# Performance work log

Measured on AMD Instinct MI355X. Metric: run time of the kernel, lower is better.

The kernel has to match this reference:

```python
import jax, jax.numpy as jnp
import numpy as np

N, K, D = 50000, 32, 128


def setup_inputs() -> dict:
    key = jax.random.key(0)
    k1, k2, k3, k4 = jax.random.split(key, 4)
    v_fea = jax.random.normal(k1, (N, D), dtype=jnp.float32)
    t_emb = jax.random.normal(k2, (N, D), dtype=jnp.float32)
    ef = jax.random.randint(k3, (N, K), 0, N, dtype=jnp.int64)
    # nn.Linear(2D, 2D, bias=False) weight, scaled like torch default init
    W = jax.random.normal(k4, (2 * D, 2 * D), dtype=jnp.float32) * (1.0 / np.sqrt(2 * D))
    return {"v_fea": v_fea, "t_emb": t_emb, "ef": ef, "W": W}


def reference(v_fea, t_emb, ef, W):
    # v: gathered neighbor features [N, K, D]
    v = v_fea[ef]
    # q: [N, 2D]; torch Linear applies x @ W.T
    q = jnp.concatenate([v_fea, t_emb], axis=-1)
    wq = q @ W.T                                   # [N, 2D]
    # k: [N, K, 2D]
    k = jnp.concatenate([v, t_emb[ef]], axis=-1)
    # per-edge score: bmm(k, wq[..., None]) -> [N, K]
    r = jnp.einsum("nkd,nd->nk", k, wq)
    r = jax.nn.softmax(r, axis=1)                  # softmax over neighbors
    # weighted sum over neighbors -> [N, D]
    ef_fea = jnp.einsum("nk,nkd->nd", r, v)
    return ef_fea
```

## Files before the change

### kernel.cpp

```cpp
#include <hip/hip_runtime.h>
#include <hip/hip_bf16.h>

#define D     128
#define TWO_D 256
#define KNB   32

typedef __attribute__((ext_vector_type(8))) short    s8;
typedef __attribute__((ext_vector_type(8))) _Float16 h8;
typedef __attribute__((ext_vector_type(2))) _Float16 h2v;
typedef __attribute__((ext_vector_type(4))) float    f4;

__device__ inline unsigned short f2h(float f) {
    return __builtin_bit_cast(unsigned short, (_Float16)f);
}
__device__ inline float h2f(unsigned short u) {
    return (float)__builtin_bit_cast(_Float16, u);
}

union v16u { s8 s; h2v h[4]; };

__device__ inline float dot8(s8 x, s8 w, float acc) {
#if __has_builtin(__builtin_amdgcn_fdot2)
    v16u ux, uw; ux.s = x; uw.s = w;
#pragma unroll
    for (int j = 0; j < 4; ++j)
        acc = __builtin_amdgcn_fdot2(ux.h[j], uw.h[j], acc, false);
#else
#pragma unroll
    for (int j = 0; j < 8; ++j)
        acc = fmaf(h2f((unsigned short)x[j]), h2f((unsigned short)w[j]), acc);
#endif
    return acc;
}

__global__ __launch_bounds__(256) void cast_kernel(
    const float* __restrict__ a, const float* __restrict__ b,
    unsigned short* __restrict__ ph, int total)
{
    int i = blockIdx.x * 256 + threadIdx.x;
    if (i >= total) return;
    int n = i >> 4, j = i & 15;
    const float4* pv = (const float4*)(a + (size_t)n * D + j * 8);
    const float4* pt = (const float4*)(b + (size_t)n * D + j * 8);
    float4 v0 = pv[0], v1 = pv[1];
    float4 t0 = pt[0], t1 = pt[1];
    s8 qv, qt;
    qv[0]=(short)f2h(v0.x); qv[1]=(short)f2h(v0.y); qv[2]=(short)f2h(v0.z); qv[3]=(short)f2h(v0.w);
    qv[4]=(short)f2h(v1.x); qv[5]=(short)f2h(v1.y); qv[6]=(short)f2h(v1.z); qv[7]=(short)f2h(v1.w);
    qt[0]=(short)f2h(t0.x); qt[1]=(short)f2h(t0.y); qt[2]=(short)f2h(t0.z); qt[3]=(short)f2h(t0.w);
    qt[4]=(short)f2h(t1.x); qt[5]=(short)f2h(t1.y); qt[6]=(short)f2h(t1.z); qt[7]=(short)f2h(t1.w);
    *(s8*)(ph + (size_t)n * TWO_D + j * 8)     = qv;
    *(s8*)(ph + (size_t)n * TWO_D + D + j * 8) = qt;
}

#define BM 128
#define BN 128
#define BK 32
#define LDT 56

__global__ __launch_bounds__(256) void gemm_wq_mfma(
    const unsigned short* __restrict__ ph,
    const float* __restrict__ W, unsigned short* __restrict__ wq_h, int M)
{
    __shared__ unsigned short As[BM][LDT];
    __shared__ unsigned short Bs[BN][LDT];

    const int tid  = threadIdx.x;
    const int w    = tid >> 6;
    const int lane = tid & 63;
    const int quad = lane >> 4;
    const int l16  = lane & 15;
    const int row0 = blockIdx.x * BM;
    const int i0   = blockIdx.y * BN;

    f4 acc[2][8] = {};

    const int srow = tid >> 1;
    const int seg  = tid & 1;
    int ga = row0 + srow; if (ga >= M) ga = M - 1;

    for (int kt = 0; kt < TWO_D; kt += BK) {
        const unsigned short* pa = ph + (size_t)ga * TWO_D + kt + seg * 16;
        s8 a0 = *(const s8*)(pa);
        s8 a1 = *(const s8*)(pa + 8);
        const float* pb = W + (size_t)(i0 + srow) * TWO_D + kt + seg * 16;
        float4 b0 = *(const float4*)(pb);
        float4 b1 = *(const float4*)(pb + 4);
        float4 b2 = *(const float4*)(pb + 8);
        float4 b3 = *(const float4*)(pb + 12);

        __syncthreads();
        *(s8*)&As[srow][seg * 16]     = a0;
        *(s8*)&As[srow][seg * 16 + 8] = a1;
        {
            s8 q0, q1;
            q0[0]=(short)f2h(b0.x); q0[1]=(short)f2h(b0.y); q0[2]=(short)f2h(b0.z); q0[3]=(short)f2h(b0.w);
            q0[4]=(short)f2h(b1.x); q0[5]=(short)f2h(b1.y); q0[6]=(short)f2h(b1.z); q0[7]=(short)f2h(b1.w);
            q1[0]=(short)f2h(b2.x); q1[1]=(short)f2h(b2.y); q1[2]=(short)f2h(b2.z); q1[3]=(short)f2h(b2.w);
            q1[4]=(short)f2h(b3.x); q1[5]=(short)f2h(b3.y); q1[6]=(short)f2h(b3.z); q1[7]=(short)f2h(b3.w);
            *(s8*)&Bs[srow][seg * 16]     = q0;
            *(s8*)&Bs[srow][seg * 16 + 8] = q1;
        }
        __syncthreads();

        s8 af0 = *(const s8*)&As[w * 32 + l16][quad * 8];
        s8 af1 = *(const s8*)&As[w * 32 + 16 + l16][quad * 8];
#pragma unroll
        for (int nt = 0; nt < 8; ++nt) {
            s8 bf = *(const s8*)&Bs[nt * 16 + l16][quad * 8];
            acc[0][nt] = __builtin_amdgcn_mfma_f32_16x16x32_f16(
                __builtin_bit_cast(h8, af0), __builtin_bit_cast(h8, bf), acc[0][nt], 0, 0, 0);
            acc[1][nt] = __builtin_amdgcn_mfma_f32_16x16x32_f16(
                __builtin_bit_cast(h8, af1), __builtin_bit_cast(h8, bf), acc[1][nt], 0, 0, 0);
        }
    }

#pragma unroll
    for (int mt = 0; mt < 2; ++mt) {
#pragma unroll
        for (int nt = 0; nt < 8; ++nt) {
#pragma unroll
            for (int r = 0; r < 4; ++r) {
                int grow = row0 + w * 32 + mt * 16 + quad * 4 + r;
                if (grow < M)
                    wq_h[(size_t)grow * TWO_D + i0 + nt * 16 + l16] = f2h(acc[mt][nt][r]);
            }
        }
    }
}

__global__ __attribute__((amdgpu_waves_per_eu(4, 4))) __launch_bounds__(256)
void attn_kernel(
    const unsigned short* __restrict__ ph, const int* __restrict__ ef,
    const unsigned short* __restrict__ wq_h, float* __restrict__ outp, int M)
{
    const int lane = threadIdx.x & 63;
    const int w    = threadIdx.x >> 6;
    const int n    = blockIdx.x * 4 + w;
    if (n >= M) return;

    const int g = lane >> 4;
    const int j = lane & 15;

    const unsigned short* wp = wq_h + (size_t)n * TWO_D + j * 16;
    s8 wqa = *(const s8*)(wp);
    s8 wqb = *(const s8*)(wp + 8);

    int eidx = 0;
    if (lane < KNB) eidx = ef[n * KNB + lane];

    s8 xa[8], xb[8];
#pragma unroll
    for (int p = 0; p < 8; ++p) {
        int e = __shfl(eidx, 4 * p + g, 64);
        const unsigned short* rp = ph + (size_t)e * TWO_D + j * 16;
        xa[p] = *(const s8*)(rp);
        xb[p] = *(const s8*)(rp + 8);
    }
    __builtin_amdgcn_sched_barrier(0);

    float s[8];
#pragma unroll
    for (int p = 0; p < 8; ++p) {
        float t = dot8(xa[p], wqa, 0.f);
        s[p] = dot8(xb[p], wqb, t);
    }

#pragma unroll
    for (int p = 0; p < 8; ++p) {
#pragma unroll
        for (int off = 8; off; off >>= 1) s[p] += __shfl_xor(s[p], off, 64);
    }
    float m = -1e30f;
#pragma unroll
    for (int p = 0; p < 8; ++p) {
        float sb = __shfl_xor(s[p], 16, 64);
        float m2 = fmaxf(s[p], sb);
        float m3 = __shfl_xor(m2, 32, 64);
        m = fmaxf(m, fmaxf(m2, m3));
    }
    float e[8];
    float psum = 0.f;
#pragma unroll
    for (int p = 0; p < 8; ++p) {
        e[p] = __expf(s[p] - m);
        psum += e[p];
    }
    psum += __shfl_xor(psum, 16, 64);
    psum += __shfl_xor(psum, 32, 64);

    float o[16] = {};
#pragma unroll
    for (int p = 0; p < 8; ++p) {
        v16u ua, ub; ua.s = xa[p]; ub.s = xb[p];
#pragma unroll
        for (int t = 0; t < 4; ++t) {
            o[2*t]     = fmaf(e[p], (float)ua.h[t][0], o[2*t]);
            o[2*t+1]   = fmaf(e[p], (float)ua.h[t][1], o[2*t+1]);
            o[8+2*t]   = fmaf(e[p], (float)ub.h[t][0], o[8+2*t]);
            o[8+2*t+1] = fmaf(e[p], (float)ub.h[t][1], o[8+2*t+1]);
        }
    }
#pragma unroll
    for (int t = 0; t < 16; ++t) {
        o[t] += __shfl_xor(o[t], 16, 64);
        o[t] += __shfl_xor(o[t], 32, 64);
    }

    if (lane < 8) {
        float inv = 1.0f / psum;
        float* orow = outp + (size_t)n * D + lane * 16;
#pragma unroll
        for (int c = 0; c < 4; ++c) {
            float4 st = make_float4(o[4*c] * inv, o[4*c+1] * inv,
                                    o[4*c+2] * inv, o[4*c+3] * inv);
            *(float4*)(orow + 4 * c) = st;
        }
    }
}

extern "C" void kernel_launch(void* const* d_in, const int* in_sizes, int n_in,
                              void* d_out, int out_size, void* d_ws, size_t ws_size,
                              hipStream_t stream)
{
    const float* v_fea = (const float*)d_in[0];
    const float* t_emb = (const float*)d_in[1];
    const int*   ef    = (const int*)d_in[2];
    const float* W     = (const float*)d_in[3];
    float* outp = (float*)d_out;

    const int M = in_sizes[0] / D;
    char* ws = (char*)d_ws;
    unsigned short* wq_h = (unsigned short*)ws;
    unsigned short* ph   = (unsigned short*)(ws + (size_t)M * TWO_D * 2);

    const int total = M * 16;
    cast_kernel<<<(total + 255) / 256, 256, 0, stream>>>(v_fea, t_emb, ph, total);

    dim3 gg((M + BM - 1) / BM, TWO_D / BN);
    gemm_wq_mfma<<<gg, 256, 0, stream>>>(ph, W, wq_h, M);
    attn_kernel<<<(M + 3) / 4, 256, 0, stream>>>(ph, ef, wq_h, outp, M);
}
```

Measured before the change: 225.0 us.

## Fuse fp16 cast into GEMM and stage neighbor gathers through LDS

Removes the separate cast kernel: the GEMM now reads fp32 v_fea/t_emb directly, packs them to fp16 for the MFMA tiles, and the y==0 blocks also write the fp16 concatenated rows used later. The attention kernel changes its lane-to-column mapping so only the v half of each gathered row goes to LDS via global_load_lds, while the t half stays in registers. The v data is then re-read from LDS for the weighted sum. This cuts register pressure, which is meant to allow the higher waves_per_eu target. It also saves a kernel launch and a full fp16 round trip through memory, at the cost of the GEMM reading twice as many bytes for A and using more LDS in attention.

```diff
diff --git a/kernel.cpp b/kernel.cpp
--- a/kernel.cpp
+++ b/kernel.cpp
@@ -33,24 +33,17 @@
     return acc;
 }
 
-__global__ __launch_bounds__(256) void cast_kernel(
-    const float* __restrict__ a, const float* __restrict__ b,
-    unsigned short* __restrict__ ph, int total)
-{
-    int i = blockIdx.x * 256 + threadIdx.x;
-    if (i >= total) return;
-    int n = i >> 4, j = i & 15;
-    const float4* pv = (const float4*)(a + (size_t)n * D + j * 8);
-    const float4* pt = (const float4*)(b + (size_t)n * D + j * 8);
-    float4 v0 = pv[0], v1 = pv[1];
-    float4 t0 = pt[0], t1 = pt[1];
-    s8 qv, qt;
-    qv[0]=(short)f2h(v0.x); qv[1]=(short)f2h(v0.y); qv[2]=(short)f2h(v0.z); qv[3]=(short)f2h(v0.w);
-    qv[4]=(short)f2h(v1.x); qv[5]=(short)f2h(v1.y); qv[6]=(short)f2h(v1.z); qv[7]=(short)f2h(v1.w);
-    qt[0]=(short)f2h(t0.x); qt[1]=(short)f2h(t0.y); qt[2]=(short)f2h(t0.z); qt[3]=(short)f2h(t0.w);
-    qt[4]=(short)f2h(t1.x); qt[5]=(short)f2h(t1.y); qt[6]=(short)f2h(t1.z); qt[7]=(short)f2h(t1.w);
-    *(s8*)(ph + (size_t)n * TWO_D + j * 8)     = qv;
-    *(s8*)(ph + (size_t)n * TWO_D + D + j * 8) = qt;
+__device__ inline void gl_lds16(const void* g, void* l) {
+    __builtin_amdgcn_global_load_lds(
+        (const __attribute__((address_space(1))) void*)g,
+        (__attribute__((address_space(3))) void*)l, 16, 0, 0);
+}
+
+__device__ inline s8 pack8(float4 x, float4 y) {
+    s8 q;
+    q[0]=(short)f2h(x.x); q[1]=(short)f2h(x.y); q[2]=(short)f2h(x.z); q[3]=(short)f2h(x.w);
+    q[4]=(short)f2h(y.x); q[5]=(short)f2h(y.y); q[6]=(short)f2h(y.z); q[7]=(short)f2h(y.w);
+    return q;
 }
 
 #define BM 128
@@ -58,9 +51,10 @@
 #define BK 32
 #define LDT 56
 
-__global__ __launch_bounds__(256) void gemm_wq_mfma(
-    const unsigned short* __restrict__ ph,
-    const float* __restrict__ W, unsigned short* __restrict__ wq_h, int M)
+__global__ __launch_bounds__(256) void gemm_cast_wq(
+    const float* __restrict__ v_fea, const float* __restrict__ t_emb,
+    const float* __restrict__ W, unsigned short* __restrict__ wq_h,
+    unsigned short* __restrict__ ph, int M)
 {
     __shared__ unsigned short As[BM][LDT];
     __shared__ unsigned short Bs[BN][LDT];
@@ -72,35 +66,40 @@
     const int l16  = lane & 15;
     const int row0 = blockIdx.x * BM;
     const int i0   = blockIdx.y * BN;
+    const bool wr_ph = (blockIdx.y == 0);
 
     f4 acc[2][8] = {};
 
     const int srow = tid >> 1;
     const int seg  = tid & 1;
-    int ga = row0 + srow; if (ga >= M) ga = M - 1;
+    const int grow_s = row0 + srow;
+    int ga = grow_s; if (ga >= M) ga = M - 1;
 
     for (int kt = 0; kt < TWO_D; kt += BK) {
-        const unsigned short* pa = ph + (size_t)ga * TWO_D + kt + seg * 16;
-        s8 a0 = *(const s8*)(pa);
-        s8 a1 = *(const s8*)(pa + 8);
+        const float* srcA = (kt < D) ? v_fea : t_emb;
+        const int kb = (kt & (D - 1)) + seg * 16;
+        const float* pa = srcA + (size_t)ga * D + kb;
+        float4 a0 = *(const float4*)(pa);
+        float4 a1 = *(const float4*)(pa + 4);
+        float4 a2 = *(const float4*)(pa + 8);
+        float4 a3 = *(const float4*)(pa + 12);
         const float* pb = W + (size_t)(i0 + srow) * TWO_D + kt + seg * 16;
         float4 b0 = *(const float4*)(pb);
         float4 b1 = *(const float4*)(pb + 4);
         float4 b2 = *(const float4*)(pb + 8);
         float4 b3 = *(const float4*)(pb + 12);
 
+        s8 A0 = pack8(a0, a1), A1 = pack8(a2, a3);
+        if (wr_ph && grow_s < M) {
+            *(s8*)(ph + (size_t)grow_s * TWO_D + kt + seg * 16)     = A0;
+            *(s8*)(ph + (size_t)grow_s * TWO_D + kt + seg * 16 + 8) = A1;
+        }
+
         __syncthreads();
-        *(s8*)&As[srow][seg * 16]     = a0;
-        *(s8*)&As[srow][seg * 16 + 8] = a1;
-        {
-            s8 q0, q1;
-            q0[0]=(short)f2h(b0.x); q0[1]=(short)f2h(b0.y); q0[2]=(short)f2h(b0.z); q0[3]=(short)f2h(b0.w);
-            q0[4]=(short)f2h(b1.x); q0[5]=(short)f2h(b1.y); q0[6]=(short)f2h(b1.z); q0[7]=(short)f2h(b1.w);
-            q1[0]=(short)f2h(b2.x); q1[1]=(short)f2h(b2.y); q1[2]=(short)f2h(b2.z); q1[3]=(short)f2h(b2.w);
-            q1[4]=(short)f2h(b3.x); q1[5]=(short)f2h(b3.y); q1[6]=(short)f2h(b3.z); q1[7]=(short)f2h(b3.w);
-            *(s8*)&Bs[srow][seg * 16]     = q0;
-            *(s8*)&Bs[srow][seg * 16 + 8] = q1;
-        }
+        *(s8*)&As[srow][seg * 16]     = A0;
+        *(s8*)&As[srow][seg * 16 + 8] = A1;
+        *(s8*)&Bs[srow][seg * 16]     = pack8(b0, b1);
+        *(s8*)&Bs[srow][seg * 16 + 8] = pack8(b2, b3);
         __syncthreads();
 
         s8 af0 = *(const s8*)&As[w * 32 + l16][quad * 8];
@@ -129,11 +128,13 @@
     }
 }
 
-__global__ __attribute__((amdgpu_waves_per_eu(4, 4))) __launch_bounds__(256)
+__global__ __attribute__((amdgpu_waves_per_eu(5, 6))) __launch_bounds__(256)
 void attn_kernel(
     const unsigned short* __restrict__ ph, const int* __restrict__ ef,
     const unsigned short* __restrict__ wq_h, float* __restrict__ outp, int M)
 {
+    __shared__ char smem[4][8192];
+
     const int lane = threadIdx.x & 63;
     const int w    = threadIdx.x >> 6;
     const int n    = blockIdx.x * 4 + w;
@@ -142,28 +143,31 @@
     const int g = lane >> 4;
     const int j = lane & 15;
 
-    const unsigned short* wp = wq_h + (size_t)n * TWO_D + j * 16;
+    const unsigned short* wp = wq_h + (size_t)n * TWO_D + j * 8;
     s8 wqa = *(const s8*)(wp);
-    s8 wqb = *(const s8*)(wp + 8);
+    s8 wqb = *(const s8*)(wp + D);
 
     int eidx = 0;
     if (lane < KNB) eidx = ef[n * KNB + lane];
 
-    s8 xa[8], xb[8];
+    char* base = smem[w];
+    s8 t8[8];
 #pragma unroll
     for (int p = 0; p < 8; ++p) {
         int e = __shfl(eidx, 4 * p + g, 64);
-        const unsigned short* rp = ph + (size_t)e * TWO_D + j * 16;
-        xa[p] = *(const s8*)(rp);
-        xb[p] = *(const s8*)(rp + 8);
-    }
+        const char* rp = (const char*)ph + (size_t)e * 512 + j * 16;
+        gl_lds16(rp, base + p * 1024);
+        t8[p] = *(const s8*)(rp + 256);
+    }
+    asm volatile("s_waitcnt vmcnt(0)" ::: "memory");
     __builtin_amdgcn_sched_barrier(0);
 
     float s[8];
 #pragma unroll
     for (int p = 0; p < 8; ++p) {
-        float t = dot8(xa[p], wqa, 0.f);
-        s[p] = dot8(xb[p], wqb, t);
+        s8 v8 = *(const s8*)(base + p * 1024 + lane * 16);
+        float t = dot8(v8, wqa, 0.f);
+        s[p] = dot8(t8[p], wqb, t);
     }
 
 #pragma unroll
@@ -189,33 +193,28 @@
     psum += __shfl_xor(psum, 16, 64);
     psum += __shfl_xor(psum, 32, 64);
 
-    float o[16] = {};
-#pragma unroll
-    for (int p = 0; p < 8; ++p) {
-        v16u ua, ub; ua.s = xa[p]; ub.s = xb[p];
+    float o[8] = {};
+#pragma unroll
+    for (int p = 0; p < 8; ++p) {
+        s8 v8 = *(const s8*)(base + p * 1024 + lane * 16);
+        v16u u; u.s = v8;
 #pragma unroll
         for (int t = 0; t < 4; ++t) {
-            o[2*t]     = fmaf(e[p], (float)ua.h[t][0], o[2*t]);
-            o[2*t+1]   = fmaf(e[p], (float)ua.h[t][1], o[2*t+1]);
-            o[8+2*t]   = fmaf(e[p], (float)ub.h[t][0], o[8+2*t]);
-            o[8+2*t+1] = fmaf(e[p], (float)ub.h[t][1], o[8+2*t+1]);
-        }
-    }
-#pragma unroll
-    for (int t = 0; t < 16; ++t) {
+            o[2*t]   = fmaf(e[p], (float)u.h[t][0], o[2*t]);
+            o[2*t+1] = fmaf(e[p], (float)u.h[t][1], o[2*t+1]);
+        }
+    }
+#pragma unroll
+    for (int t = 0; t < 8; ++t) {
         o[t] += __shfl_xor(o[t], 16, 64);
         o[t] += __shfl_xor(o[t], 32, 64);
     }
 
-    if (lane < 8) {
+    if (lane < 16) {
         float inv = 1.0f / psum;
-        float* orow = outp + (size_t)n * D + lane * 16;
-#pragma unroll
-        for (int c = 0; c < 4; ++c) {
-            float4 st = make_float4(o[4*c] * inv, o[4*c+1] * inv,
-                                    o[4*c+2] * inv, o[4*c+3] * inv);
-            *(float4*)(orow + 4 * c) = st;
-        }
+        float* orow = outp + (size_t)n * D + j * 8;
+        *(float4*)(orow)     = make_float4(o[0]*inv, o[1]*inv, o[2]*inv, o[3]*inv);
+        *(float4*)(orow + 4) = make_float4(o[4]*inv, o[5]*inv, o[6]*inv, o[7]*inv);
     }
 }
 
@@ -234,10 +233,7 @@
     unsigned short* wq_h = (unsigned short*)ws;
     unsigned short* ph   = (unsigned short*)(ws + (size_t)M * TWO_D * 2);
 
-    const int total = M * 16;
-    cast_kernel<<<(total + 255) / 256, 256, 0, stream>>>(v_fea, t_emb, ph, total);
-
     dim3 gg((M + BM - 1) / BM, TWO_D / BN);
-    gemm_wq_mfma<<<gg, 256, 0, stream>>>(ph, W, wq_h, M);
+    gemm_cast_wq<<<gg, 256, 0, stream>>>(v_fea, t_emb, W, wq_h, ph, M);
     attn_kernel<<<(M + 3) / 4, 256, 0, stream>>>(ph, ef, wq_h, outp, M);
 }
```

Result: no change. 222.9 us (-0.9%).
